# Optimization experiments

Measured on AMD Instinct MI355X. Metric: run time of the kernel, lower is better.

## Reference

```python
import jax, jax.numpy as jnp
import numpy as np

N_Q = 50000
B, T = 256, 500
DK = 128      # q_embed_dim == memory_key_state_dim == final_fc_dim
DV = 256      # qa_embed_dim == memory_value_state_dim
M = 50        # memory_size

def setup_inputs() -> dict:
    key = jax.random.key(0)
    ks = jax.random.split(key, 12)
    q_data = jax.random.randint(ks[0], (B, T), 0, N_Q + 1)
    qa_data = jax.random.randint(ks[1], (B, T), 0, 2 * N_Q + 1)
    # target in {-1, 0, 1}; -1 = padding (masked out)
    u = jax.random.uniform(ks[2], (B * T, 1))
    target = jnp.floor(u * 3.0) - 1.0
    # embedding tables with padding_idx=0 zeroed
    q_tab = (jax.random.normal(ks[3], (N_Q + 1, DK)) * (2.0 / DK) ** 0.5).at[0].set(0.0)
    qa_tab = (jax.random.normal(ks[4], (2 * N_Q + 1, DV)) * (2.0 / DV) ** 0.5).at[0].set(0.0)
    Mk = jax.random.normal(ks[5], (M, DK)) * (2.0 / DK) ** 0.5
    Mv0 = jax.random.normal(ks[6], (M, DV)) * (2.0 / DV) ** 0.5
    We = jax.random.normal(ks[7], (DV, DV)) * (1.0 / DV) ** 0.5
    be = jnp.zeros((DV,))
    Wa = jax.random.normal(ks[8], (DV, DV)) * (1.0 / DV) ** 0.5
    ba = jnp.zeros((DV,))
    Wr = jax.random.normal(ks[9], (DK, DV + DK)) * (2.0 / (DV + DK)) ** 0.5
    br = jnp.zeros((DK,))
    Wp = jax.random.normal(ks[10], (1, DK)) * (2.0 / DK) ** 0.5
    bp = jnp.zeros((1,))
    return dict(q_data=q_data, qa_data=qa_data, target=target, q_tab=q_tab,
                qa_tab=qa_tab, Mk=Mk, Mv0=Mv0, We=We, be=be, Wa=Wa, ba=ba,
                Wr=Wr, br=br, Wp=Wp, bp=bp)


def reference(q_data, qa_data, target, q_tab, qa_tab, Mk, Mv0, We, be, Wa, ba, Wr, br, Wp, bp):
    b, t = q_data.shape
    q_e = q_tab[q_data]            # (B,T,DK)
    qa_e = qa_tab[qa_data]         # (B,T,DV)
    wr_mask = (q_data >= 1).astype(q_e.dtype)  # write gate per step
    Mv_init = jnp.broadcast_to(Mv0[None], (b, M, DV))

    def step(Mv, xs):
        q, qa, m = xs              # q:(B,DK) qa:(B,DV) m:(B,)
        w = jax.nn.softmax(q @ Mk.T, axis=-1)          # (B,M) correlation weight
        read = jnp.einsum('bm,bmd->bd', w, Mv)         # (B,DV)
        e = jax.nn.sigmoid(qa @ We.T + be)             # erase (B,DV)
        a = jnp.tanh(qa @ Wa.T + ba)                   # add   (B,DV)
        new = Mv * (1.0 - w[:, :, None] * e[:, None, :]) + w[:, :, None] * a[:, None, :]
        Mv = jnp.where(m[:, None, None] > 0, new, Mv)  # only write for non-pad steps
        return Mv, read

    _, reads = jax.lax.scan(step, Mv_init,
                            (q_e.transpose(1, 0, 2), qa_e.transpose(1, 0, 2), wr_mask.T))
    reads = reads.transpose(1, 0, 2)                    # (B,T,DV)
    feat = jnp.concatenate([reads, q_e], axis=2).reshape(b * t, DV + DK)
    h = jnp.tanh(feat @ Wr.T + br)                      # (B*T,DK)
    pred = h @ Wp.T + bp                                # (B*T,1) logits
    mask = target >= 0
    # stable BCE-with-logits per element
    per = jnp.maximum(pred, 0.0) - pred * target + jnp.log1p(jnp.exp(-jnp.abs(pred)))
    n_valid = jnp.maximum(jnp.sum(mask.astype(pred.dtype)), 1.0)
    loss = jnp.sum(jnp.where(mask, per, 0.0)) / n_valid
    probs = jax.nn.sigmoid(pred)
    return loss, probs
```

## Files before the change

### kernel.cpp

```cpp
#include <hip/hip_runtime.h>
#include <hip/hip_bf16.h>
#include <stdint.h>


#define BATCH 256
#define TLEN  500
#define DKQ   128
#define DVV   256
#define MSZ   50
#define NROWS 128000
#define GSZ   10

__device__ __forceinline__ float bfs(uint16_t u){
  union { uint32_t u; float f; } v; v.u = ((uint32_t)u) << 16; return v.f;
}
__device__ __forceinline__ uint16_t f2b(float x){
  union { __hip_bfloat16 h; uint16_t u; } c; c.h = __float2bfloat16(x); return c.u;
}

typedef __attribute__((ext_vector_type(8))) short bf16x8;
typedef __attribute__((ext_vector_type(4))) float f32x4;

__device__ __forceinline__ void gl_lds16(const void* g, void* l){
  __builtin_amdgcn_global_load_lds(
      (const __attribute__((address_space(1))) void*)g,
      (__attribute__((address_space(3))) void*)l, 16, 0, 0);
}

__global__ __launch_bounds__(128, 1) void k_w(
    const int* __restrict__ q_data, const float* __restrict__ q_tab,
    const float* __restrict__ Mk, float* __restrict__ w_ws)
{
  __shared__ float mk[MSZ*DKQ];
  __shared__ float wt[128*52];
  const int tid = threadIdx.x;
  for (int li = tid; li < 1600; li += 128)
    ((float4*)mk)[li] = ((const float4*)Mk)[li];
  __syncthreads();

  const int row = blockIdx.x*128 + tid;
  const int qi = q_data[row];
  const float4* qrow = (const float4*)(q_tab + (size_t)qi*DKQ);

  float acc[MSZ];
  #pragma unroll
  for (int m=0;m<MSZ;m++) acc[m] = 0.f;

  #pragma unroll 1
  for (int c8=0; c8<8; c8++){
    float4 q0 = qrow[c8*4+0], q1 = qrow[c8*4+1], q2 = qrow[c8*4+2], q3 = qrow[c8*4+3];
    #pragma unroll
    for (int m=0;m<MSZ;m++){
      const float4* mr = (const float4*)&mk[m*DKQ + c8*16];
      float4 a = mr[0], b = mr[1], cc = mr[2], d = mr[3];
      float s = acc[m];
      s = fmaf(q0.x,a.x,s);  s = fmaf(q0.y,a.y,s);  s = fmaf(q0.z,a.z,s);  s = fmaf(q0.w,a.w,s);
      s = fmaf(q1.x,b.x,s);  s = fmaf(q1.y,b.y,s);  s = fmaf(q1.z,b.z,s);  s = fmaf(q1.w,b.w,s);
      s = fmaf(q2.x,cc.x,s); s = fmaf(q2.y,cc.y,s); s = fmaf(q2.z,cc.z,s); s = fmaf(q2.w,cc.w,s);
      s = fmaf(q3.x,d.x,s);  s = fmaf(q3.y,d.y,s);  s = fmaf(q3.z,d.z,s);  s = fmaf(q3.w,d.w,s);
      acc[m] = s;
    }
  }
  float mx = acc[0];
  #pragma unroll
  for (int m=1;m<MSZ;m++) mx = fmaxf(mx, acc[m]);
  float s = 0.f;
  #pragma unroll
  for (int m=0;m<MSZ;m++){ acc[m] = __expf(acc[m]-mx); s += acc[m]; }
  float inv = 1.0f / s;
  #pragma unroll
  for (int m=0;m<MSZ;m++) wt[tid*52+m] = acc[m]*inv;
  wt[tid*52+50] = 0.f; wt[tid*52+51] = 0.f;
  __syncthreads();
  float4* dst = (float4*)(w_ws + (size_t)blockIdx.x*128*52);
  const float4* src = (const float4*)wt;
  for (int li = tid; li < 1664; li += 128) dst[li] = src[li];
}

__global__ __launch_bounds__(256) void k_cvt(
    const float* __restrict__ qa_tab, const float* __restrict__ We,
    const float* __restrict__ Wa, uint16_t* __restrict__ qa_bf,
    uint16_t* __restrict__ wcomb)
{
  const size_t n_qa4 = 6400064;
  const size_t n_w4  = 32768;
  size_t stride = (size_t)gridDim.x*blockDim.x;
  for (size_t i = (size_t)blockIdx.x*256 + threadIdx.x; i < n_qa4 + n_w4; i += stride){
    float4 v;
    if (i < n_qa4){
      v = ((const float4*)qa_tab)[i];
      ushort4 o; o.x=f2b(v.x); o.y=f2b(v.y); o.z=f2b(v.z); o.w=f2b(v.w);
      ((ushort4*)qa_bf)[i] = o;
    } else {
      size_t j = i - n_qa4;
      size_t f = j*4;
      int col = (int)(f >> 8), k = (int)(f & 255);
      const float* srcp = (col < 256) ? (We + (size_t)col*256 + k)
                                      : (Wa + (size_t)(col-256)*256 + k);
      v = *(const float4*)srcp;
      ushort4 o; o.x=f2b(v.x); o.y=f2b(v.y); o.z=f2b(v.z); o.w=f2b(v.w);
      ((ushort4*)wcomb)[j] = o;
    }
  }
}

__global__ __launch_bounds__(256) void k_cvt2(
    const float* __restrict__ q_tab, const float* __restrict__ Wr,
    uint16_t* __restrict__ q_bf, uint16_t* __restrict__ wr_bf)
{
  const size_t n_q4  = 1600032;
  const size_t n_wr4 = 12288;
  size_t stride = (size_t)gridDim.x*blockDim.x;
  for (size_t i = (size_t)blockIdx.x*256 + threadIdx.x; i < n_q4 + n_wr4; i += stride){
    if (i < n_q4){
      float4 v = ((const float4*)q_tab)[i];
      ushort4 o; o.x=f2b(v.x); o.y=f2b(v.y); o.z=f2b(v.z); o.w=f2b(v.w);
      ((ushort4*)q_bf)[i] = o;
    } else {
      size_t j = i - n_q4;
      float4 v = ((const float4*)Wr)[j];
      ushort4 o; o.x=f2b(v.x); o.y=f2b(v.y); o.z=f2b(v.z); o.w=f2b(v.w);
      ((ushort4*)wr_bf)[j] = o;
    }
  }
}

__global__ __launch_bounds__(256, 2) void k_ea(
    const int* __restrict__ qa_data, const uint16_t* __restrict__ qa_bf,
    const uint16_t* __restrict__ wcomb, const float* __restrict__ be,
    const float* __restrict__ ba, __hip_bfloat16* __restrict__ ea_ws)
{
  __shared__ uint16_t Ab[128*32];
  __shared__ uint16_t Bb[128*32];
  const int tid = threadIdx.x;
  const int lane = tid & 63, wid = tid >> 6;
  const int braw = blockIdx.x;
  const int nb = (braw >> 3) & 3;
  const int mb = (braw & 7) | ((braw >> 5) << 3);
  const int rb = mb*128, cb = nb*128;

  const char* qac = (const char*)qa_bf;
  size_t aoff0, aoff1;
  {
    int r0 = wid*32 + (lane>>2);
    aoff0 = (size_t)qa_data[rb + r0]*512      + (size_t)(lane&3)*16;
    aoff1 = (size_t)qa_data[rb + r0 + 16]*512 + (size_t)(lane&3)*16;
  }
  const char* wcb = (const char*)wcomb;
  size_t boff0 = (size_t)(cb + wid*32 + (lane>>2))*512 + (size_t)(lane&3)*16;
  size_t boff1 = boff0 + 16*512;

  const int wr = (wid>>1)*64, wc = (wid&1)*64;
  float bias[4];
  #pragma unroll
  for (int tj=0;tj<4;tj++){
    int colg = cb + wc + tj*16 + (lane&15);
    bias[tj] = (nb<2) ? be[colg] : ba[colg-256];
  }

  f32x4 acc[4][4];
  #pragma unroll
  for (int i=0;i<4;i++){
    #pragma unroll
    for (int j=0;j<4;j++) acc[i][j] = (f32x4)(0.f);
  }

  #pragma unroll 1
  for (int kc=0; kc<8; kc++){
    __syncthreads();
    gl_lds16(qac + aoff0 + (size_t)kc*64, &Ab[(wid*2+0)*512]);
    gl_lds16(qac + aoff1 + (size_t)kc*64, &Ab[(wid*2+1)*512]);
    gl_lds16(wcb + boff0 + (size_t)kc*64, &Bb[(wid*2+0)*512]);
    gl_lds16(wcb + boff1 + (size_t)kc*64, &Bb[(wid*2+1)*512]);
    __syncthreads();
    bf16x8 af[4], bfr[4];
    #pragma unroll
    for (int ti=0;ti<4;ti++)
      af[ti] = *(const bf16x8*)&Ab[(wr + ti*16 + (lane&15))*32 + (lane>>4)*8];
    #pragma unroll
    for (int tj=0;tj<4;tj++)
      bfr[tj] = *(const bf16x8*)&Bb[(wc + tj*16 + (lane&15))*32 + (lane>>4)*8];
    #pragma unroll
    for (int ti=0;ti<4;ti++){
      #pragma unroll
      for (int tj=0;tj<4;tj++)
        acc[ti][tj] = __builtin_amdgcn_mfma_f32_16x16x32_bf16(af[ti], bfr[tj], acc[ti][tj], 0, 0, 0);
    }
  }
  const int rq = (lane>>4)*4, cl = lane&15;
  #pragma unroll
  for (int ti=0;ti<4;ti++){
    #pragma unroll
    for (int r=0;r<4;r++){
      int row = rb + wr + ti*16 + rq + r;
      __hip_bfloat16* orow = ea_ws + (size_t)row*512 + cb + wc;
      #pragma unroll
      for (int tj=0;tj<4;tj++){
        float x = acc[ti][tj][r] + bias[tj];
        float v = (nb<2) ? (1.f/(1.f+__expf(-x)))
                         : (1.f - 2.f/(__expf(2.f*x)+1.f));
        orow[tj*16 + cl] = __float2bfloat16(v);
      }
    }
  }
}

__global__ __launch_bounds__(512, 1) void k_scan(
    const int* __restrict__ q_data, const float* __restrict__ w_ws,
    const uint16_t* __restrict__ ea_ws, const float* __restrict__ Mv0,
    __hip_bfloat16* __restrict__ reads_ws)
{
  __shared__ float wbuf[2][GSZ*52];
  __shared__ float part[2][256];
  const int tid = threadIdx.x;
  const int d = tid & 255, h = tid >> 8;
  const int base = blockIdx.x*TLEN;

  float Mv[28];
  #pragma unroll
  for (int qq=0; qq<7; qq++){
    #pragma unroll
    for (int e=0;e<4;e++){
      int quad = 2*qq + h, m = quad*4 + e;
      Mv[qq*4+e] = (quad <= 12 && m < MSZ) ? Mv0[m*256 + d] : 0.f;
    }
  }

  float4 wreg;
  uint16_t ecur[GSZ], acur[GSZ], enxt[GSZ], anxt[GSZ];
  int qcur[GSZ], qnxt[GSZ];

  if (tid < 130) wreg = ((const float4*)(w_ws + (size_t)base*52))[tid];
  #pragma unroll
  for (int j=0;j<GSZ;j++){
    ecur[j] = ea_ws[(size_t)(base+j)*512 + d];
    acur[j] = ea_ws[(size_t)(base+j)*512 + 256 + d];
    qcur[j] = q_data[base+j];
  }
  if (tid < 130) ((float4*)wbuf[0])[tid] = wreg;
  __syncthreads();

  #pragma unroll 1
  for (int g=0; g<50; g++){
    if (g < 49){
      const int sn = base + (g+1)*GSZ;
      if (tid < 130) wreg = ((const float4*)(w_ws + (size_t)sn*52))[tid];
      #pragma unroll
      for (int j=0;j<GSZ;j++){
        enxt[j] = ea_ws[(size_t)(sn+j)*512 + d];
        anxt[j] = ea_ws[(size_t)(sn+j)*512 + 256 + d];
        qnxt[j] = q_data[sn+j];
      }
    }
    const float* wb = wbuf[g&1];
    const int s0 = base + g*GSZ;
    #pragma unroll
    for (int j=0;j<GSZ;j++){
      const float4* wq = (const float4*)(wb + j*52);
      float ef = bfs(ecur[j]), af = bfs(acur[j]);
      float4 wv[7];
      #pragma unroll
      for (int qq=0; qq<6; qq++) wv[qq] = wq[2*qq + h];
      if (h == 0) wv[6] = wq[12];
      float r0=0.f, r1=0.f, r2=0.f, r3=0.f;
      #pragma unroll
      for (int qq=0; qq<6; qq++){
        r0 = fmaf(wv[qq].x, Mv[qq*4+0], r0);
        r1 = fmaf(wv[qq].y, Mv[qq*4+1], r1);
        r2 = fmaf(wv[qq].z, Mv[qq*4+2], r2);
        r3 = fmaf(wv[qq].w, Mv[qq*4+3], r3);
      }
      if (h == 0){
        r0 = fmaf(wv[6].x, Mv[24], r0);
        r1 = fmaf(wv[6].y, Mv[25], r1);
        r2 = fmaf(wv[6].z, Mv[26], r2);
        r3 = fmaf(wv[6].w, Mv[27], r3);
      }
      float rp = (r0+r1)+(r2+r3);
      if (h == 0) part[j&1][d] = rp;
      __syncthreads();
      if (h == 1){
        float rd = rp + part[j&1][d];
        reads_ws[(size_t)(s0+j)*256 + d] = __float2bfloat16(rd);
      }
      if (qcur[j] > 0){
        #pragma unroll
        for (int qq=0; qq<6; qq++){
          { float tt = fmaf(ef, Mv[qq*4+0], -af); Mv[qq*4+0] = fmaf(-wv[qq].x, tt, Mv[qq*4+0]); }
          { float tt = fmaf(ef, Mv[qq*4+1], -af); Mv[qq*4+1] = fmaf(-wv[qq].y, tt, Mv[qq*4+1]); }
          { float tt = fmaf(ef, Mv[qq*4+2], -af); Mv[qq*4+2] = fmaf(-wv[qq].z, tt, Mv[qq*4+2]); }
          { float tt = fmaf(ef, Mv[qq*4+3], -af); Mv[qq*4+3] = fmaf(-wv[qq].w, tt, Mv[qq*4+3]); }
        }
        if (h == 0){
          { float tt = fmaf(ef, Mv[24], -af); Mv[24] = fmaf(-wv[6].x, tt, Mv[24]); }
          { float tt = fmaf(ef, Mv[25], -af); Mv[25] = fmaf(-wv[6].y, tt, Mv[25]); }
        }
      }
    }
    if (g < 49){
      if (tid < 130) ((float4*)wbuf[(g+1)&1])[tid] = wreg;
      #pragma unroll
      for (int j=0;j<GSZ;j++){ ecur[j]=enxt[j]; acur[j]=anxt[j]; qcur[j]=qnxt[j]; }
    }
    __syncthreads();
  }
}

__global__ __launch_bounds__(256, 2) void k_final(
    const int* __restrict__ q_data, const uint16_t* __restrict__ q_bf,
    const uint16_t* __restrict__ reads16, const uint16_t* __restrict__ wr_bf,
    const float* __restrict__ br, const float* __restrict__ Wp,
    const float* __restrict__ bp, const float* __restrict__ target,
    float* __restrict__ out, float* __restrict__ parts)
{
  __shared__ uint16_t Ab[64*32];
  __shared__ uint16_t Bb[128*32];
  __shared__ float redbuf[8];
  const int tid = threadIdx.x;
  const int lane = tid & 63, wid = tid >> 6;
  const int rb = blockIdx.x * 64;

  const char* rdc = (const char*)reads16;
  const char* qbc = (const char*)q_bf;
  const char* wrc = (const char*)wr_bf;
  const int arow = wid*16 + (lane>>2);
  size_t aoff_r = (size_t)(rb+arow)*512 + (size_t)(lane&3)*16;
  size_t aoff_q = (size_t)q_data[rb+arow]*256 + (size_t)(lane&3)*16;
  size_t boff0  = (size_t)(wid*32 + (lane>>2))*768 + (size_t)(lane&3)*16;
  size_t boff1  = boff0 + 16*768;

  f32x4 acc[8];
  #pragma unroll
  for (int tj=0;tj<8;tj++) acc[tj] = (f32x4)(0.f);

  #pragma unroll 1
  for (int kc=0; kc<12; kc++){
    __syncthreads();
    if (kc < 8) gl_lds16(rdc + aoff_r + (size_t)kc*64,     &Ab[wid*512]);
    else        gl_lds16(qbc + aoff_q + (size_t)(kc-8)*64, &Ab[wid*512]);
    gl_lds16(wrc + boff0 + (size_t)kc*64, &Bb[(wid*2+0)*512]);
    gl_lds16(wrc + boff1 + (size_t)kc*64, &Bb[(wid*2+1)*512]);
    __syncthreads();
    bf16x8 af = *(const bf16x8*)&Ab[(wid*16 + (lane&15))*32 + (lane>>4)*8];
    #pragma unroll
    for (int tj=0;tj<8;tj++){
      bf16x8 bf = *(const bf16x8*)&Bb[(tj*16 + (lane&15))*32 + (lane>>4)*8];
      acc[tj] = __builtin_amdgcn_mfma_f32_16x16x32_bf16(af, bf, acc[tj], 0, 0, 0);
    }
  }
  const int cl = lane & 15, rq = lane >> 4;
  float p[4] = {0.f,0.f,0.f,0.f};
  #pragma unroll
  for (int tj=0;tj<8;tj++){
    int cg = tj*16 + cl;
    float brv = br[cg], wpv = Wp[cg];
    #pragma unroll
    for (int r=0;r<4;r++){
      float x = acc[tj][r] + brv;
      float hh = 1.f - 2.f/(__expf(2.f*x)+1.f);
      p[r] = fmaf(hh, wpv, p[r]);
    }
  }
  #pragma unroll
  for (int off=1; off<16; off<<=1){
    #pragma unroll
    for (int r=0;r<4;r++) p[r] += __shfl_xor(p[r], off);
  }
  float bpv = bp[0];
  float lsum = 0.f, csum = 0.f;
  if (cl == 0){
    #pragma unroll
    for (int r=0;r<4;r++){
      int row = rb + wid*16 + rq*4 + r;
      float pred = p[r] + bpv;
      out[1 + row] = 1.f/(1.f + __expf(-pred));
      float tg = target[row];
      if (tg >= 0.f){
        lsum += fmaxf(pred, 0.f) - pred*tg + log1pf(__expf(-fabsf(pred)));
        csum += 1.f;
      }
    }
  }
  #pragma unroll
  for (int off=16; off<64; off<<=1){
    lsum += __shfl_xor(lsum, off);
    csum += __shfl_xor(csum, off);
  }
  if (lane == 0){ redbuf[wid*2] = lsum; redbuf[wid*2+1] = csum; }
  __syncthreads();
  if (tid == 0){
    parts[blockIdx.x]        = redbuf[0]+redbuf[2]+redbuf[4]+redbuf[6];
    parts[2000 + blockIdx.x] = redbuf[1]+redbuf[3]+redbuf[5]+redbuf[7];
  }
}

__global__ __launch_bounds__(256) void k_loss(
    const float* __restrict__ parts, float* __restrict__ out)
{
  __shared__ float red[8];
  const int tid = threadIdx.x;
  float l = 0.f, cn = 0.f;
  for (int i = tid; i < 2000; i += 256){ l += parts[i]; cn += parts[2000+i]; }
  #pragma unroll
  for (int off=32; off>0; off>>=1){ l += __shfl_xor(l, off); cn += __shfl_xor(cn, off); }
  if ((tid & 63) == 0){ red[(tid>>6)*2] = l; red[(tid>>6)*2+1] = cn; }
  __syncthreads();
  if (tid == 0){
    float L = red[0]+red[2]+red[4]+red[6];
    float C = red[1]+red[3]+red[5]+red[7];
    out[0] = L / fmaxf(C, 1.f);
  }
}

extern "C" void kernel_launch(void* const* d_in, const int* in_sizes, int n_in,
                              void* d_out, int out_size, void* d_ws, size_t ws_size,
                              hipStream_t stream) {
  const int*   q_data  = (const int*)d_in[0];
  const int*   qa_data = (const int*)d_in[1];
  const float* target  = (const float*)d_in[2];
  const float* q_tab   = (const float*)d_in[3];
  const float* qa_tab  = (const float*)d_in[4];
  const float* Mk  = (const float*)d_in[5];
  const float* Mv0 = (const float*)d_in[6];
  const float* We  = (const float*)d_in[7];
  const float* be  = (const float*)d_in[8];
  const float* Wa  = (const float*)d_in[9];
  const float* ba  = (const float*)d_in[10];
  const float* Wr  = (const float*)d_in[11];
  const float* br  = (const float*)d_in[12];
  const float* Wp  = (const float*)d_in[13];
  const float* bp  = (const float*)d_in[14];

  char* ws = (char*)d_ws;
  float*          w_ws     = (float*)ws;
  __hip_bfloat16* ea_ws    = (__hip_bfloat16*)(ws + 26624000);
  uint16_t*       qa_bf    = (uint16_t*)(ws + 157696000);
  uint16_t*       wcomb    = (uint16_t*)(ws + 208896512);
  __hip_bfloat16* reads_ws = (__hip_bfloat16*)(ws + 157696000);
  float*          parts    = (float*)ws;
  uint16_t*       q_bf     = (uint16_t*)(ws + 2000000);
  uint16_t*       wr_bf    = (uint16_t*)(ws + 16000000);

  float* out = (float*)d_out;

  k_w    <<<1000, 128, 0, stream>>>(q_data, q_tab, Mk, w_ws);
  k_cvt  <<<2048, 256, 0, stream>>>(qa_tab, We, Wa, qa_bf, wcomb);
  k_ea   <<<4000, 256, 0, stream>>>(qa_data, qa_bf, wcomb, be, ba, ea_ws);
  k_scan <<<256,  512, 0, stream>>>(q_data, w_ws, (const uint16_t*)ea_ws, Mv0, reads_ws);
  k_cvt2 <<<1024, 256, 0, stream>>>(q_tab, Wr, q_bf, wr_bf);
  k_final<<<2000, 256, 0, stream>>>(q_data, q_bf, (const uint16_t*)reads_ws, wr_bf, br, Wp, bp, target, out, parts);
  k_loss <<<1,    256, 0, stream>>>(parts, out);
}
```

Measured before the change: 644.1 us.

## Split scan over memory slots within a wave and drop block barriers

```diff
diff --git a/kernel.cpp b/kernel.cpp
--- a/kernel.cpp
+++ b/kernel.cpp
@@ -205,104 +205,103 @@
   }
 }
 
-__global__ __launch_bounds__(512, 1) void k_scan(
+__global__ __launch_bounds__(512, 4) void k_scan(
     const int* __restrict__ q_data, const float* __restrict__ w_ws,
     const uint16_t* __restrict__ ea_ws, const float* __restrict__ Mv0,
     __hip_bfloat16* __restrict__ reads_ws)
 {
-  __shared__ float wbuf[2][GSZ*52];
-  __shared__ float part[2][256];
-  const int tid = threadIdx.x;
-  const int d = tid & 255, h = tid >> 8;
-  const int base = blockIdx.x*TLEN;
-
-  float Mv[28];
-  #pragma unroll
-  for (int qq=0; qq<7; qq++){
-    #pragma unroll
-    for (int e=0;e<4;e++){
-      int quad = 2*qq + h, m = quad*4 + e;
-      Mv[qq*4+e] = (quad <= 12 && m < MSZ) ? Mv0[m*256 + d] : 0.f;
-    }
-  }
-
-  float4 wreg;
-  uint16_t ecur[GSZ], acur[GSZ], enxt[GSZ], anxt[GSZ];
-  int qcur[GSZ], qnxt[GSZ];
-
-  if (tid < 130) wreg = ((const float4*)(w_ws + (size_t)base*52))[tid];
+  const int tid  = threadIdx.x;
+  const int bid  = blockIdx.x;
+  const int b    = bid & 255;
+  const int dblk = bid >> 8;
+  const int lane = tid & 63;
+  const int h    = lane >> 4;
+  const int d    = dblk*128 + (tid >> 6)*16 + (lane & 15);
+  const int base = b * TLEN;
+
+  float Mv[16];
+  #pragma unroll
+  for (int k=0;k<3;k++){
+    #pragma unroll
+    for (int e=0;e<4;e++)
+      Mv[k*4+e] = Mv0[(size_t)((4*k+h)*4+e)*256 + d];
+  }
+  #pragma unroll
+  for (int e=0;e<4;e++)
+    Mv[12+e] = (h==0 && (48+e)<MSZ) ? Mv0[(size_t)(48+e)*256 + d] : 0.f;
+
+  uint32_t epk[GSZ], epn[GSZ];
+  int qc[GSZ], qn[GSZ];
   #pragma unroll
   for (int j=0;j<GSZ;j++){
-    ecur[j] = ea_ws[(size_t)(base+j)*512 + d];
-    acur[j] = ea_ws[(size_t)(base+j)*512 + 256 + d];
-    qcur[j] = q_data[base+j];
-  }
-  if (tid < 130) ((float4*)wbuf[0])[tid] = wreg;
-  __syncthreads();
+    uint32_t e16 = ea_ws[(size_t)(base+j)*512 + d];
+    uint32_t a16 = ea_ws[(size_t)(base+j)*512 + 256 + d];
+    epk[j] = (a16 << 16) | e16;
+    qc[j]  = __builtin_amdgcn_readfirstlane(q_data[base+j]);
+  }
+  float4 w0, w1, w2, w3;
+  {
+    const float4* wq = (const float4*)(w_ws + (size_t)base*52);
+    w0 = wq[h]; w1 = wq[4+h]; w2 = wq[8+h]; w3 = wq[12];
+  }
 
   #pragma unroll 1
   for (int g=0; g<50; g++){
     if (g < 49){
       const int sn = base + (g+1)*GSZ;
-      if (tid < 130) wreg = ((const float4*)(w_ws + (size_t)sn*52))[tid];
       #pragma unroll
       for (int j=0;j<GSZ;j++){
-        enxt[j] = ea_ws[(size_t)(sn+j)*512 + d];
-        anxt[j] = ea_ws[(size_t)(sn+j)*512 + 256 + d];
-        qnxt[j] = q_data[sn+j];
+        uint32_t e16 = ea_ws[(size_t)(sn+j)*512 + d];
+        uint32_t a16 = ea_ws[(size_t)(sn+j)*512 + 256 + d];
+        epn[j] = (a16 << 16) | e16;
+        qn[j]  = __builtin_amdgcn_readfirstlane(q_data[sn+j]);
       }
     }
-    const float* wb = wbuf[g&1];
     const int s0 = base + g*GSZ;
     #pragma unroll
     for (int j=0;j<GSZ;j++){
-      const float4* wq = (const float4*)(wb + j*52);
-      float ef = bfs(ecur[j]), af = bfs(acur[j]);
-      float4 wv[7];
-      #pragma unroll
-      for (int qq=0; qq<6; qq++) wv[qq] = wq[2*qq + h];
-      if (h == 0) wv[6] = wq[12];
+      int tn = g*GSZ + j + 1; if (tn > TLEN-1) tn = TLEN-1;
+      const float4* wqn = (const float4*)(w_ws + (size_t)(base+tn)*52);
+      float4 n0 = wqn[h], n1 = wqn[4+h], n2 = wqn[8+h], n3 = wqn[12];
+
+      const uint32_t p = epk[j];
+      union { uint32_t u; float f; } ue, ua;
+      ue.u = p << 16; ua.u = p & 0xffff0000u;
+      const float ef = ue.f, af = ua.f;
+
       float r0=0.f, r1=0.f, r2=0.f, r3=0.f;
-      #pragma unroll
-      for (int qq=0; qq<6; qq++){
-        r0 = fmaf(wv[qq].x, Mv[qq*4+0], r0);
-        r1 = fmaf(wv[qq].y, Mv[qq*4+1], r1);
-        r2 = fmaf(wv[qq].z, Mv[qq*4+2], r2);
-        r3 = fmaf(wv[qq].w, Mv[qq*4+3], r3);
-      }
+      r0 = fmaf(w0.x, Mv[0],  r0);  r1 = fmaf(w0.y, Mv[1],  r1);
+      r2 = fmaf(w0.z, Mv[2],  r2);  r3 = fmaf(w0.w, Mv[3],  r3);
+      r0 = fmaf(w1.x, Mv[4],  r0);  r1 = fmaf(w1.y, Mv[5],  r1);
+      r2 = fmaf(w1.z, Mv[6],  r2);  r3 = fmaf(w1.w, Mv[7],  r3);
+      r0 = fmaf(w2.x, Mv[8],  r0);  r1 = fmaf(w2.y, Mv[9],  r1);
+      r2 = fmaf(w2.z, Mv[10], r2);  r3 = fmaf(w2.w, Mv[11], r3);
       if (h == 0){
-        r0 = fmaf(wv[6].x, Mv[24], r0);
-        r1 = fmaf(wv[6].y, Mv[25], r1);
-        r2 = fmaf(wv[6].z, Mv[26], r2);
-        r3 = fmaf(wv[6].w, Mv[27], r3);
+        r0 = fmaf(w3.x, Mv[12], r0);  r1 = fmaf(w3.y, Mv[13], r1);
+        r2 = fmaf(w3.z, Mv[14], r2);  r3 = fmaf(w3.w, Mv[15], r3);
       }
       float rp = (r0+r1)+(r2+r3);
-      if (h == 0) part[j&1][d] = rp;
-      __syncthreads();
-      if (h == 1){
-        float rd = rp + part[j&1][d];
-        reads_ws[(size_t)(s0+j)*256 + d] = __float2bfloat16(rd);
+      float rs = rp + __shfl_xor(rp, 16);
+      rs += __shfl_xor(rs, 32);
+      if (h == 0)
+        reads_ws[(size_t)(s0+j)*256 + d] = __float2bfloat16(rs);
+
+      if (qc[j] > 0){
+        #define UPD(W, I) { float tt = fmaf(ef, Mv[I], -af); Mv[I] = fmaf(-(W), tt, Mv[I]); }
+        UPD(w0.x,0)  UPD(w0.y,1)  UPD(w0.z,2)  UPD(w0.w,3)
+        UPD(w1.x,4)  UPD(w1.y,5)  UPD(w1.z,6)  UPD(w1.w,7)
+        UPD(w2.x,8)  UPD(w2.y,9)  UPD(w2.z,10) UPD(w2.w,11)
+        if (h == 0){
+          UPD(w3.x,12) UPD(w3.y,13) UPD(w3.z,14) UPD(w3.w,15)
+        }
+        #undef UPD
       }
-      if (qcur[j] > 0){
-        #pragma unroll
-        for (int qq=0; qq<6; qq++){
-          { float tt = fmaf(ef, Mv[qq*4+0], -af); Mv[qq*4+0] = fmaf(-wv[qq].x, tt, Mv[qq*4+0]); }
-          { float tt = fmaf(ef, Mv[qq*4+1], -af); Mv[qq*4+1] = fmaf(-wv[qq].y, tt, Mv[qq*4+1]); }
-          { float tt = fmaf(ef, Mv[qq*4+2], -af); Mv[qq*4+2] = fmaf(-wv[qq].z, tt, Mv[qq*4+2]); }
-          { float tt = fmaf(ef, Mv[qq*4+3], -af); Mv[qq*4+3] = fmaf(-wv[qq].w, tt, Mv[qq*4+3]); }
-        }
-        if (h == 0){
-          { float tt = fmaf(ef, Mv[24], -af); Mv[24] = fmaf(-wv[6].x, tt, Mv[24]); }
-          { float tt = fmaf(ef, Mv[25], -af); Mv[25] = fmaf(-wv[6].y, tt, Mv[25]); }
-        }
-      }
+      w0 = n0; w1 = n1; w2 = n2; w3 = n3;
     }
     if (g < 49){
-      if (tid < 130) ((float4*)wbuf[(g+1)&1])[tid] = wreg;
       #pragma unroll
-      for (int j=0;j<GSZ;j++){ ecur[j]=enxt[j]; acur[j]=anxt[j]; qcur[j]=qnxt[j]; }
-    }
-    __syncthreads();
+      for (int j=0;j<GSZ;j++){ epk[j] = epn[j]; qc[j] = qn[j]; }
+    }
   }
 }
 
@@ -446,7 +445,7 @@
   k_w    <<<1000, 128, 0, stream>>>(q_data, q_tab, Mk, w_ws);
   k_cvt  <<<2048, 256, 0, stream>>>(qa_tab, We, Wa, qa_bf, wcomb);
   k_ea   <<<4000, 256, 0, stream>>>(qa_data, qa_bf, wcomb, be, ba, ea_ws);
-  k_scan <<<256,  512, 0, stream>>>(q_data, w_ws, (const uint16_t*)ea_ws, Mv0, reads_ws);
+  k_scan <<<512,  512, 0, stream>>>(q_data, w_ws, (const uint16_t*)ea_ws, Mv0, reads_ws);
   k_cvt2 <<<1024, 256, 0, stream>>>(q_tab, Wr, q_bf, wr_bf);
   k_final<<<2000, 256, 0, stream>>>(q_data, q_bf, (const uint16_t*)reads_ws, wr_bf, br, Wp, bp, target, out, parts);
   k_loss <<<1,    256, 0, stream>>>(parts, out);
```

New measurement: 725.7 us. 12.7% more time.

## Split scan over value-dim halves and read weights via scalar loads

Applied to the files above, without the earlier changes.

```diff
diff --git a/kernel.cpp b/kernel.cpp
--- a/kernel.cpp
+++ b/kernel.cpp
@@ -205,104 +205,110 @@
   }
 }
 
-__global__ __launch_bounds__(512, 1) void k_scan(
+__global__ __launch_bounds__(256, 2) void k_scan(
     const int* __restrict__ q_data, const float* __restrict__ w_ws,
     const uint16_t* __restrict__ ea_ws, const float* __restrict__ Mv0,
     __hip_bfloat16* __restrict__ reads_ws)
 {
-  __shared__ float wbuf[2][GSZ*52];
-  __shared__ float part[2][256];
-  const int tid = threadIdx.x;
-  const int d = tid & 255, h = tid >> 8;
-  const int base = blockIdx.x*TLEN;
+  __shared__ float part[2][128];
+  const int tid  = threadIdx.x;
+  const int dl   = tid & 127;
+  const int h    = tid >> 7;
+  const int b    = blockIdx.x & 255;
+  const int dblk = blockIdx.x >> 8;
+  const int d    = dblk*128 + dl;
+  const int base = b * TLEN;
+  const int f0   = __builtin_amdgcn_readfirstlane(h * 28);
 
   float Mv[28];
   #pragma unroll
-  for (int qq=0; qq<7; qq++){
-    #pragma unroll
-    for (int e=0;e<4;e++){
-      int quad = 2*qq + h, m = quad*4 + e;
-      Mv[qq*4+e] = (quad <= 12 && m < MSZ) ? Mv0[m*256 + d] : 0.f;
-    }
-  }
-
-  float4 wreg;
+  for (int i=0;i<28;i++){
+    int m = f0 + i;
+    Mv[i] = (m < MSZ) ? Mv0[(size_t)m*256 + d] : 0.f;
+  }
+
+  typedef const __attribute__((address_space(4))) float  cfloat;
+  typedef const __attribute__((address_space(4))) f32x4  cf32x4;
+  typedef const __attribute__((address_space(4))) int    cint;
+  cfloat* wbase = (cfloat*)w_ws + (size_t)base*52 + f0;
+  cint*   qbase = (cint*)q_data + base;
+
+  f32x4 wc[7], wn[7];
+  #pragma unroll
+  for (int qq=0; qq<7; qq++) wc[qq] = ((cf32x4*)wbase)[qq];
+
   uint16_t ecur[GSZ], acur[GSZ], enxt[GSZ], anxt[GSZ];
-  int qcur[GSZ], qnxt[GSZ];
-
-  if (tid < 130) wreg = ((const float4*)(w_ws + (size_t)base*52))[tid];
   #pragma unroll
   for (int j=0;j<GSZ;j++){
     ecur[j] = ea_ws[(size_t)(base+j)*512 + d];
     acur[j] = ea_ws[(size_t)(base+j)*512 + 256 + d];
-    qcur[j] = q_data[base+j];
-  }
-  if (tid < 130) ((float4*)wbuf[0])[tid] = wreg;
-  __syncthreads();
+  }
 
   #pragma unroll 1
   for (int g=0; g<50; g++){
     if (g < 49){
       const int sn = base + (g+1)*GSZ;
-      if (tid < 130) wreg = ((const float4*)(w_ws + (size_t)sn*52))[tid];
       #pragma unroll
       for (int j=0;j<GSZ;j++){
         enxt[j] = ea_ws[(size_t)(sn+j)*512 + d];
         anxt[j] = ea_ws[(size_t)(sn+j)*512 + 256 + d];
-        qnxt[j] = q_data[sn+j];
-      }
-    }
-    const float* wb = wbuf[g&1];
+      }
+    }
+    int qv[GSZ];
+    #pragma unroll
+    for (int j=0;j<GSZ;j++) qv[j] = qbase[g*GSZ + j];
     const int s0 = base + g*GSZ;
+
     #pragma unroll
     for (int j=0;j<GSZ;j++){
-      const float4* wq = (const float4*)(wb + j*52);
-      float ef = bfs(ecur[j]), af = bfs(acur[j]);
-      float4 wv[7];
-      #pragma unroll
-      for (int qq=0; qq<6; qq++) wv[qq] = wq[2*qq + h];
-      if (h == 0) wv[6] = wq[12];
+      int tn = g*GSZ + j + 1; if (tn > TLEN-1) tn = TLEN-1;
+      cf32x4* wq = (cf32x4*)(wbase + (size_t)tn*52);
+      #pragma unroll
+      for (int qq=0; qq<7; qq++) wn[qq] = wq[qq];
+
+      const float ef = bfs(ecur[j]), af = bfs(acur[j]);
       float r0=0.f, r1=0.f, r2=0.f, r3=0.f;
       #pragma unroll
       for (int qq=0; qq<6; qq++){
-        r0 = fmaf(wv[qq].x, Mv[qq*4+0], r0);
-        r1 = fmaf(wv[qq].y, Mv[qq*4+1], r1);
-        r2 = fmaf(wv[qq].z, Mv[qq*4+2], r2);
-        r3 = fmaf(wv[qq].w, Mv[qq*4+3], r3);
+        r0 = fmaf(wc[qq].x, Mv[qq*4+0], r0);
+        r1 = fmaf(wc[qq].y, Mv[qq*4+1], r1);
+        r2 = fmaf(wc[qq].z, Mv[qq*4+2], r2);
+        r3 = fmaf(wc[qq].w, Mv[qq*4+3], r3);
       }
       if (h == 0){
-        r0 = fmaf(wv[6].x, Mv[24], r0);
-        r1 = fmaf(wv[6].y, Mv[25], r1);
-        r2 = fmaf(wv[6].z, Mv[26], r2);
-        r3 = fmaf(wv[6].w, Mv[27], r3);
+        r0 = fmaf(wc[6].x, Mv[24], r0);
+        r1 = fmaf(wc[6].y, Mv[25], r1);
+        r2 = fmaf(wc[6].z, Mv[26], r2);
+        r3 = fmaf(wc[6].w, Mv[27], r3);
       }
       float rp = (r0+r1)+(r2+r3);
-      if (h == 0) part[j&1][d] = rp;
+      if (h == 0) part[j&1][dl] = rp;
       __syncthreads();
-      if (h == 1){
-        float rd = rp + part[j&1][d];
-        reads_ws[(size_t)(s0+j)*256 + d] = __float2bfloat16(rd);
-      }
-      if (qcur[j] > 0){
+      if (h == 1)
+        reads_ws[(size_t)(s0+j)*256 + d] = __float2bfloat16(rp + part[j&1][dl]);
+
+      if (qv[j] > 0){
         #pragma unroll
         for (int qq=0; qq<6; qq++){
-          { float tt = fmaf(ef, Mv[qq*4+0], -af); Mv[qq*4+0] = fmaf(-wv[qq].x, tt, Mv[qq*4+0]); }
-          { float tt = fmaf(ef, Mv[qq*4+1], -af); Mv[qq*4+1] = fmaf(-wv[qq].y, tt, Mv[qq*4+1]); }
-          { float tt = fmaf(ef, Mv[qq*4+2], -af); Mv[qq*4+2] = fmaf(-wv[qq].z, tt, Mv[qq*4+2]); }
-          { float tt = fmaf(ef, Mv[qq*4+3], -af); Mv[qq*4+3] = fmaf(-wv[qq].w, tt, Mv[qq*4+3]); }
+          { float tt = fmaf(ef, Mv[qq*4+0], -af); Mv[qq*4+0] = fmaf(-wc[qq].x, tt, Mv[qq*4+0]); }
+          { float tt = fmaf(ef, Mv[qq*4+1], -af); Mv[qq*4+1] = fmaf(-wc[qq].y, tt, Mv[qq*4+1]); }
+          { float tt = fmaf(ef, Mv[qq*4+2], -af); Mv[qq*4+2] = fmaf(-wc[qq].z, tt, Mv[qq*4+2]); }
+          { float tt = fmaf(ef, Mv[qq*4+3], -af); Mv[qq*4+3] = fmaf(-wc[qq].w, tt, Mv[qq*4+3]); }
         }
         if (h == 0){
-          { float tt = fmaf(ef, Mv[24], -af); Mv[24] = fmaf(-wv[6].x, tt, Mv[24]); }
-          { float tt = fmaf(ef, Mv[25], -af); Mv[25] = fmaf(-wv[6].y, tt, Mv[25]); }
+          { float tt = fmaf(ef, Mv[24], -af); Mv[24] = fmaf(-wc[6].x, tt, Mv[24]); }
+          { float tt = fmaf(ef, Mv[25], -af); Mv[25] = fmaf(-wc[6].y, tt, Mv[25]); }
+          { float tt = fmaf(ef, Mv[26], -af); Mv[26] = fmaf(-wc[6].z, tt, Mv[26]); }
+          { float tt = fmaf(ef, Mv[27], -af); Mv[27] = fmaf(-wc[6].w, tt, Mv[27]); }
         }
       }
+      #pragma unroll
+      for (int qq=0; qq<7; qq++) wc[qq] = wn[qq];
     }
     if (g < 49){
-      if (tid < 130) ((float4*)wbuf[(g+1)&1])[tid] = wreg;
-      #pragma unroll
-      for (int j=0;j<GSZ;j++){ ecur[j]=enxt[j]; acur[j]=anxt[j]; qcur[j]=qnxt[j]; }
-    }
-    __syncthreads();
+      #pragma unroll
+      for (int j=0;j<GSZ;j++){ ecur[j]=enxt[j]; acur[j]=anxt[j]; }
+    }
   }
 }
 
@@ -446,7 +452,7 @@
   k_w    <<<1000, 128, 0, stream>>>(q_data, q_tab, Mk, w_ws);
   k_cvt  <<<2048, 256, 0, stream>>>(qa_tab, We, Wa, qa_bf, wcomb);
   k_ea   <<<4000, 256, 0, stream>>>(qa_data, qa_bf, wcomb, be, ba, ea_ws);
-  k_scan <<<256,  512, 0, stream>>>(q_data, w_ws, (const uint16_t*)ea_ws, Mv0, reads_ws);
+  k_scan <<<512,  256, 0, stream>>>(q_data, w_ws, (const uint16_t*)ea_ws, Mv0, reads_ws);
   k_cvt2 <<<1024, 256, 0, stream>>>(q_tab, Wr, q_bf, wr_bf);
   k_final<<<2000, 256, 0, stream>>>(q_data, q_bf, (const uint16_t*)reads_ws, wr_bf, br, Wp, bp, target, out, parts);
   k_loss <<<1,    256, 0, stream>>>(parts, out);
```

Result: slower. 752.6 us (+16.8%).
